# Kernel optimization log

Measured on AMD Instinct MI355X. Metric: run time of the kernel, lower is better.

## Reference

```python
import jax, jax.numpy as jnp
import numpy as np

N, C, S = 2, 512, 256
SCALE = 2.0

def setup_inputs() -> dict:
    key = jax.random.key(0)
    kq, kk, kv = jax.random.split(key, 3)
    q = jax.random.normal(kq, (N, C, S), dtype=jnp.float32)
    k = jax.random.normal(kk, (N, C, S), dtype=jnp.float32)
    v = jax.random.normal(kv, (N, C, S), dtype=jnp.float32)
    return {"q": q, "k": k, "v": v}

def reference(q, k, v):
    # q: (N,C,S) -> (N,C,1,S); k: (N,C,S) -> (N,1,C,S)
    # weights[n,c,d] = -sum_s |k[n,d,s] - q[n,c,s]| / scale
    diff = jnp.abs(k[:, None, :, :] - q[:, :, None, :])  # (N,C,C,S)
    weights = -(diff / SCALE).sum(axis=-1)               # (N,C,C)
    weights = jax.nn.softmax(weights, axis=-1)
    rep = jnp.einsum('ncd,nds->ncs', weights, v)         # (N,C,S)
    return rep
```

## Files before the change

### kernel.cpp

```cpp
#include <hip/hip_runtime.h>


constexpr int N_  = 2;
constexpr int C_  = 512;
constexpr int S_  = 256;
constexpr int TC  = 4;
constexpr int NT  = 512;
constexpr int NW  = NT / 64;
constexpr int SC  = 32;
constexpr int NCH = S_ / SC;

template <int CTRL, int ROW_MASK>
__device__ __forceinline__ float dpp_add(float x) {
    int yi = __builtin_amdgcn_update_dpp(0, __float_as_int(x), CTRL, ROW_MASK, 0xf, true);
    return x + __int_as_float(yi);
}
template <int CTRL, int ROW_MASK>
__device__ __forceinline__ float dpp_max(float x) {
    int yi = __builtin_amdgcn_update_dpp(__float_as_int(x), __float_as_int(x), CTRL, ROW_MASK, 0xf, false);
    return fmaxf(x, __int_as_float(yi));
}
__device__ __forceinline__ float wave_sum_bcast(float x) {
    x = dpp_add<0x111, 0xf>(x);
    x = dpp_add<0x112, 0xf>(x);
    x = dpp_add<0x114, 0xf>(x);
    x = dpp_add<0x118, 0xf>(x);
    x = dpp_add<0x142, 0xa>(x);
    x = dpp_add<0x143, 0xc>(x);
    return __int_as_float(__builtin_amdgcn_readlane(__float_as_int(x), 63));
}
__device__ __forceinline__ float wave_max_bcast(float x) {
    x = dpp_max<0x111, 0xf>(x);
    x = dpp_max<0x112, 0xf>(x);
    x = dpp_max<0x114, 0xf>(x);
    x = dpp_max<0x118, 0xf>(x);
    x = dpp_max<0x142, 0xa>(x);
    x = dpp_max<0x143, 0xc>(x);
    return __int_as_float(__builtin_amdgcn_readlane(__float_as_int(x), 63));
}
__device__ __forceinline__ void fma4(float4& a, const float s, const float4& v) {
    a.x += s * v.x; a.y += s * v.y; a.z += s * v.z; a.w += s * v.w;
}

__global__ __launch_bounds__(NT, 1)
void laplace_attn_fused(const float* __restrict__ qg,
                        const float* __restrict__ kg,
                        const float* __restrict__ vg,
                        float* __restrict__ out) {
    __shared__ __align__(16) float  wt[C_][TC];
    __shared__ __align__(16) float4 po[NW][TC][S_ / 4];
    __shared__ float4 red1[NW];
    __shared__ float4 red2[NW];

    const int b    = blockIdx.x;
    const int n    = b & 1;
    const int c0   = (b >> 1) * TC;
    const int tid  = threadIdx.x;
    const int w    = tid >> 6;
    const int lane = tid & 63;

    const float* kn = kg + (size_t)n * C_ * S_;
    const float* vn = vg + (size_t)n * C_ * S_;
    const float* qn = qg + ((size_t)n * C_ + c0) * S_;
    const float* kd = kn + (size_t)tid * S_;

    float dist0 = 0.f, dist1 = 0.f, dist2 = 0.f, dist3 = 0.f;

    for (int ch = 0; ch < NCH; ++ch) {
        const float* q0 = qn + 0 * S_ + ch * SC;
        const float* q1 = qn + 1 * S_ + ch * SC;
        const float* q2 = qn + 2 * S_ + ch * SC;
        const float* q3 = qn + 3 * S_ + ch * SC;
        const float* kc = kd + ch * SC;
        #pragma unroll
        for (int s4 = 0; s4 < SC / 4; ++s4) {
            const float4 kf = *(const float4*)(kc + (s4 << 2));
            const int s = s4 << 2;
            dist0 += (fabsf(kf.x - q0[s]) + fabsf(kf.y - q0[s + 1]))
                   + (fabsf(kf.z - q0[s + 2]) + fabsf(kf.w - q0[s + 3]));
            dist1 += (fabsf(kf.x - q1[s]) + fabsf(kf.y - q1[s + 1]))
                   + (fabsf(kf.z - q1[s + 2]) + fabsf(kf.w - q1[s + 3]));
            dist2 += (fabsf(kf.x - q2[s]) + fabsf(kf.y - q2[s + 1]))
                   + (fabsf(kf.z - q2[s + 2]) + fabsf(kf.w - q2[s + 3]));
            dist3 += (fabsf(kf.x - q3[s]) + fabsf(kf.y - q3[s + 1]))
                   + (fabsf(kf.z - q3[s + 2]) + fabsf(kf.w - q3[s + 3]));
        }
    }

    float4 x;
    x.x = -0.5f * dist0; x.y = -0.5f * dist1;
    x.z = -0.5f * dist2; x.w = -0.5f * dist3;

    float4 mx;
    mx.x = wave_max_bcast(x.x); mx.y = wave_max_bcast(x.y);
    mx.z = wave_max_bcast(x.z); mx.w = wave_max_bcast(x.w);
    if (lane == 0) red1[w] = mx;
    __syncthreads();
    float4 M = red1[0];
    #pragma unroll
    for (int u = 1; u < NW; ++u) {
        const float4 r = red1[u];
        M.x = fmaxf(M.x, r.x); M.y = fmaxf(M.y, r.y);
        M.z = fmaxf(M.z, r.z); M.w = fmaxf(M.w, r.w);
    }

    float4 p;
    p.x = __expf(x.x - M.x); p.y = __expf(x.y - M.y);
    p.z = __expf(x.z - M.z); p.w = __expf(x.w - M.w);

    float4 sv;
    sv.x = wave_sum_bcast(p.x); sv.y = wave_sum_bcast(p.y);
    sv.z = wave_sum_bcast(p.z); sv.w = wave_sum_bcast(p.w);
    if (lane == 0) red2[w] = sv;
    __syncthreads();
    float4 L = red2[0];
    #pragma unroll
    for (int u = 1; u < NW; ++u) {
        const float4 r = red2[u];
        L.x += r.x; L.y += r.y; L.z += r.z; L.w += r.w;
    }
    p.x *= (1.f / L.x); p.y *= (1.f / L.y);
    p.z *= (1.f / L.z); p.w *= (1.f / L.w);
    *(float4*)&wt[tid][0] = p;
    __syncthreads();

    float4 o0 = make_float4(0.f, 0.f, 0.f, 0.f), o1 = o0, o2 = o0, o3 = o0;
    const int dbase = w << 6;
    #pragma unroll 8
    for (int dd = 0; dd < 64; ++dd) {
        const int d = dbase + dd;
        const float4 vv = *(const float4*)(vn + (size_t)d * S_ + (lane << 2));
        const float4 pw = *(const float4*)&wt[d][0];
        fma4(o0, pw.x, vv); fma4(o1, pw.y, vv);
        fma4(o2, pw.z, vv); fma4(o3, pw.w, vv);
    }
    po[w][0][lane] = o0; po[w][1][lane] = o1;
    po[w][2][lane] = o2; po[w][3][lane] = o3;
    __syncthreads();

    if (tid < TC * 64) {
        const int c    = tid >> 6;
        const int quad = tid & 63;
        float4 s = po[0][c][quad];
        #pragma unroll
        for (int u = 1; u < NW; ++u) {
            const float4 r = po[u][c][quad];
            s.x += r.x; s.y += r.y; s.z += r.z; s.w += r.w;
        }
        *(float4*)(out + ((size_t)n * C_ + c0 + c) * S_ + (quad << 2)) = s;
    }
}

extern "C" void kernel_launch(void* const* d_in, const int* in_sizes, int n_in,
                              void* d_out, int out_size, void* d_ws, size_t ws_size,
                              hipStream_t stream) {
    const float* q = (const float*)d_in[0];
    const float* k = (const float*)d_in[1];
    const float* v = (const float*)d_in[2];
    float* out = (float*)d_out;
    (void)d_ws; (void)ws_size;

    laplace_attn_fused<<<dim3(N_ * (C_ / TC)), dim3(NT), 0, stream>>>(q, k, v, out);
}
```

Baseline: 82.28 us.

## Stage K chunks in LDS with coalesced, double-buffered loads and a swizzle

Previously each thread read its own K row straight from global memory with strided float4 loads. Now the whole block loads each 32-column K chunk cooperatively with coalesced loads into a double-buffered LDS tile, using a rotating swizzle so later per-row reads avoid bank conflicts. The four Q rows are also staged in LDS, and the next chunk is prefetched into registers while the current one is processed. This adds a block-wide barrier per chunk and about 140KB of LDS, and reuses the K buffer for the partial-output reduction.

```diff
diff --git a/kernel.cpp b/kernel.cpp
--- a/kernel.cpp
+++ b/kernel.cpp
@@ -8,7 +8,9 @@
 constexpr int NT  = 512;
 constexpr int NW  = NT / 64;
 constexpr int SC  = 32;
+constexpr int SCQ = SC / 4;
 constexpr int NCH = S_ / SC;
+constexpr int KF  = C_ * SCQ / NT;
 
 template <int CTRL, int ROW_MASK>
 __device__ __forceinline__ float dpp_add(float x) {
@@ -47,10 +49,12 @@
                         const float* __restrict__ kg,
                         const float* __restrict__ vg,
                         float* __restrict__ out) {
-    __shared__ __align__(16) float  wt[C_][TC];
-    __shared__ __align__(16) float4 po[NW][TC][S_ / 4];
+    __shared__ __align__(16) float ksm[2][C_][SC];
+    __shared__ __align__(16) float qs[TC][S_];
+    __shared__ __align__(16) float wt[C_][TC];
     __shared__ float4 red1[NW];
     __shared__ float4 red2[NW];
+    float4 (*po)[TC][S_ / 4] = (float4 (*)[TC][S_ / 4])&ksm[0][0][0];
 
     const int b    = blockIdx.x;
     const int n    = b & 1;
@@ -62,29 +66,70 @@
     const float* kn = kg + (size_t)n * C_ * S_;
     const float* vn = vg + (size_t)n * C_ * S_;
     const float* qn = qg + ((size_t)n * C_ + c0) * S_;
-    const float* kd = kn + (size_t)tid * S_;
+
+    if (tid < TC * (S_ / 4)) {
+        const int row = tid >> 6;
+        const int col = (tid & 63) << 2;
+        *(float4*)&qs[row][col] = *(const float4*)(qn + (size_t)row * S_ + col);
+    }
+
+    const int srow = tid >> 3;
+    const int sqo  = tid & 7;
+    const int sp   = (sqo + srow) & 7;
+
+    float4 greg[KF];
+    #pragma unroll
+    for (int it = 0; it < KF; ++it) {
+        const int row = srow + (it << 6);
+        greg[it] = *(const float4*)(kn + (size_t)row * S_ + (sqo << 2));
+    }
+    #pragma unroll
+    for (int it = 0; it < KF; ++it) {
+        const int row = srow + (it << 6);
+        *(float4*)&ksm[0][row][sp << 2] = greg[it];
+    }
+    __syncthreads();
 
     float dist0 = 0.f, dist1 = 0.f, dist2 = 0.f, dist3 = 0.f;
+    int cur = 0;
 
     for (int ch = 0; ch < NCH; ++ch) {
-        const float* q0 = qn + 0 * S_ + ch * SC;
-        const float* q1 = qn + 1 * S_ + ch * SC;
-        const float* q2 = qn + 2 * S_ + ch * SC;
-        const float* q3 = qn + 3 * S_ + ch * SC;
-        const float* kc = kd + ch * SC;
+        if (ch + 1 < NCH) {
+            const float* kc = kn + (ch + 1) * SC;
+            #pragma unroll
+            for (int it = 0; it < KF; ++it) {
+                const int row = srow + (it << 6);
+                greg[it] = *(const float4*)(kc + (size_t)row * S_ + (sqo << 2));
+            }
+        }
+        const int sb = ch * SC;
         #pragma unroll
-        for (int s4 = 0; s4 < SC / 4; ++s4) {
-            const float4 kf = *(const float4*)(kc + (s4 << 2));
-            const int s = s4 << 2;
-            dist0 += (fabsf(kf.x - q0[s]) + fabsf(kf.y - q0[s + 1]))
-                   + (fabsf(kf.z - q0[s + 2]) + fabsf(kf.w - q0[s + 3]));
-            dist1 += (fabsf(kf.x - q1[s]) + fabsf(kf.y - q1[s + 1]))
-                   + (fabsf(kf.z - q1[s + 2]) + fabsf(kf.w - q1[s + 3]));
-            dist2 += (fabsf(kf.x - q2[s]) + fabsf(kf.y - q2[s + 1]))
-                   + (fabsf(kf.z - q2[s + 2]) + fabsf(kf.w - q2[s + 3]));
-            dist3 += (fabsf(kf.x - q3[s]) + fabsf(kf.y - q3[s + 1]))
-                   + (fabsf(kf.z - q3[s + 2]) + fabsf(kf.w - q3[s + 3]));
-        }
+        for (int j = 0; j < SCQ; ++j) {
+            const int p = (j + tid) & 7;
+            const float4 kf = *(const float4*)&ksm[cur][tid][p << 2];
+            const int s = sb + (j << 2);
+            const float4 qa = *(const float4*)&qs[0][s];
+            const float4 qb = *(const float4*)&qs[1][s];
+            const float4 qc = *(const float4*)&qs[2][s];
+            const float4 qd = *(const float4*)&qs[3][s];
+            dist0 += (fabsf(kf.x - qa.x) + fabsf(kf.y - qa.y))
+                   + (fabsf(kf.z - qa.z) + fabsf(kf.w - qa.w));
+            dist1 += (fabsf(kf.x - qb.x) + fabsf(kf.y - qb.y))
+                   + (fabsf(kf.z - qb.z) + fabsf(kf.w - qb.w));
+            dist2 += (fabsf(kf.x - qc.x) + fabsf(kf.y - qc.y))
+                   + (fabsf(kf.z - qc.z) + fabsf(kf.w - qc.w));
+            dist3 += (fabsf(kf.x - qd.x) + fabsf(kf.y - qd.y))
+                   + (fabsf(kf.z - qd.z) + fabsf(kf.w - qd.w));
+        }
+        if (ch + 1 < NCH) {
+            #pragma unroll
+            for (int it = 0; it < KF; ++it) {
+                const int row = srow + (it << 6);
+                *(float4*)&ksm[cur ^ 1][row][sp << 2] = greg[it];
+            }
+            cur ^= 1;
+        }
+        __syncthreads();
     }
 
     float4 x;
```

Measured after the change: 81.12 us. No clear change (-1.4%).
